# Kernel tuning notes

Hardware: AMD Instinct MI355X
Metric: run time of the kernel (lower is better)

Reference implementation:

```python
import jax, jax.numpy as jnp
import numpy as np


def setup_inputs() -> dict:
    key = jax.random.key(0)
    ks = jax.random.split(key, 10)
    N, CZ, CH = 512, 128, 128
    s = 1.0 / np.sqrt(CZ)  # keep pre-sigmoid activations in a sane range
    return {
        "z": jax.random.normal(ks[0], (N, N, CZ), dtype=jnp.float32),
        "mask": jnp.ones((N, N, 1), dtype=jnp.float32),
        "weight_ag": jax.random.normal(ks[1], (CH, CZ), dtype=jnp.float32) * s,
        "bias_ag": jax.random.normal(ks[2], (CH,), dtype=jnp.float32) * 0.02,
        "weight_ap": jax.random.normal(ks[3], (CH, CZ), dtype=jnp.float32) * s,
        "bias_ap": jax.random.normal(ks[4], (CH,), dtype=jnp.float32) * 0.02,
        "weight_bg": jax.random.normal(ks[5], (CH, CZ), dtype=jnp.float32) * s,
        "bias_bg": jax.random.normal(ks[6], (CH,), dtype=jnp.float32) * 0.02,
        "weight_bp": jax.random.normal(ks[7], (CH, CZ), dtype=jnp.float32) * s,
        "bias_bp": jax.random.normal(ks[8], (CH,), dtype=jnp.float32) * 0.02,
        "chunk_size": 32,
    }


def _triangle_mul(z, mask, w_ag, b_ag, w_ap, b_ap, w_bg, b_bg, w_bp, b_bp):
    # z: [N, N, c_z]; mask: [N, N, 1]; weights: [c, c_z]
    # a = mask * sigmoid(Linear_ag(z)) * Linear_ap(z)   -> [N, N, c]
    a = mask * jax.nn.sigmoid(jnp.einsum("ijz,cz->ijc", z, w_ag) + b_ag) * (
        jnp.einsum("ijz,cz->ijc", z, w_ap) + b_ap
    )
    b = mask * jax.nn.sigmoid(jnp.einsum("ijz,cz->ijc", z, w_bg) + b_bg) * (
        jnp.einsum("ijz,cz->ijc", z, w_bp) + b_bp
    )
    # outgoing triangle multiplicative combination, channel-first output [c, N, N]
    return jnp.einsum("ikc,jkc->cij", a, b)


def reference(z, mask, weight_ag, bias_ag, weight_ap, bias_ap,
              weight_bg, bias_bg, weight_bp, bias_bp, chunk_size):
    # The torch wrapper chunks the hidden-channel dim of the weights and
    # concatenates the per-chunk [c, N, N] outputs along dim 0. Since every
    # channel is independent, this is mathematically identical to running the
    # full computation at once; we do that (clean, fused form).
    return _triangle_mul(z, mask, weight_ag, bias_ag, weight_ap, bias_ap,
                         weight_bg, bias_bg, weight_bp, bias_bp)
```

## Files before the change

kernel.cpp:

```cpp
#include <hip/hip_runtime.h>
#include <stdint.h>


#define NDIM 512
#define CZ   128
#define CH   128
#define NPOS (NDIM * NDIM)
#define NTILE 16
#define POSB  (NTILE * 32)

typedef __attribute__((ext_vector_type(8))) __bf16 bf16x8;
typedef __attribute__((ext_vector_type(4))) float  f32x4;

__device__ __forceinline__ unsigned short f2bf(float f) {
  unsigned int u = __builtin_bit_cast(unsigned int, f);
  unsigned int r = (u + 0x7fffu + ((u >> 16) & 1u)) >> 16;
  return (unsigned short)r;
}

__global__ __launch_bounds__(256) void conv_weights(
    const float* __restrict__ wag, const float* __restrict__ wap,
    const float* __restrict__ wbg, const float* __restrict__ wbp,
    unsigned short* __restrict__ wbf) {
  int idx = blockIdx.x * 256 + threadIdx.x;
  int proj = idx >> 14;
  int rem  = idx & 16383;
  const float* src = (proj == 0) ? wag : (proj == 1) ? wap : (proj == 2) ? wbg : wbp;
  wbf[idx] = f2bf(src[rem]);
}

__global__ __launch_bounds__(256, 3) void proj_fuse(
    const float* __restrict__ z,
    const float* __restrict__ mask,
    const unsigned short* __restrict__ wbf,
    const float* __restrict__ bias_ag, const float* __restrict__ bias_ap,
    const float* __restrict__ bias_bg, const float* __restrict__ bias_bp,
    unsigned short* __restrict__ a_ws,
    unsigned short* __restrict__ b_ws) {
  __shared__ unsigned short zbuf[2][32 * 136];

  const int t    = threadIdx.x;
  const int lane = t & 63;
  const int w    = t >> 6;
  const int pair = blockIdx.y;
  const int base = blockIdx.x * POSB;

  const int ml    = lane & 15;
  const int q     = lane >> 4;
  const int koffl = q * 8;
  const int pg = pair * 2, pp = pg + 1;

  bf16x8 wg[4][2], wp[4][2];
#pragma unroll
  for (int ks = 0; ks < 4; ++ks)
#pragma unroll
    for (int ni = 0; ni < 2; ++ni) {
      const int c = w * 32 + ni * 16 + ml;
      wg[ks][ni] = *(const bf16x8*)&wbf[((size_t)pg * CH + c) * CZ + ks * 32 + koffl];
      wp[ks][ni] = *(const bf16x8*)&wbf[((size_t)pp * CH + c) * CZ + ks * 32 + koffl];
    }

  const float* bgp = pair ? bias_bg : bias_ag;
  const float* bpp = pair ? bias_bp : bias_ap;
  float bg[2], bp[2];
#pragma unroll
  for (int ni = 0; ni < 2; ++ni) {
    bg[ni] = bgp[w * 32 + ni * 16 + ml];
    bp[ni] = bpp[w * 32 + ni * 16 + ml];
  }
  unsigned short* plane = pair ? b_ws : a_ws;

  auto STAGE = [&](int b, int tt) {
    const int m0s = base + tt * 32;
#pragma unroll
    for (int it = 0; it < 4; ++it) {
      const int id  = it * 256 + t;
      const int row = id >> 5;
      const int c4  = id & 31;
      const float4 v = *(const float4*)(z + (size_t)(m0s + row) * CZ + c4 * 4);
      unsigned int lo = (unsigned int)f2bf(v.x) | ((unsigned int)f2bf(v.y) << 16);
      unsigned int hi = (unsigned int)f2bf(v.z) | ((unsigned int)f2bf(v.w) << 16);
      *(uint2*)&zbuf[b][row * 136 + c4 * 4] = make_uint2(lo, hi);
    }
  };

  STAGE(0, 0);
  __syncthreads();

#pragma unroll 1
  for (int tt = 0; tt < NTILE; ++tt) {
    const int m0 = base + tt * 32;
    const int cb = tt & 1;
    if (tt + 1 < NTILE) STAGE(cb ^ 1, tt + 1);

    f32x4 ag_[2][2], ap_[2][2];
#pragma unroll
    for (int mi = 0; mi < 2; ++mi)
#pragma unroll
      for (int ni = 0; ni < 2; ++ni) {
        ag_[mi][ni] = (f32x4){0.f, 0.f, 0.f, 0.f};
        ap_[mi][ni] = (f32x4){0.f, 0.f, 0.f, 0.f};
      }

#pragma unroll
    for (int ks = 0; ks < 4; ++ks) {
      bf16x8 af0 = *(const bf16x8*)&zbuf[cb][(ml)      * 136 + ks * 32 + koffl];
      bf16x8 af1 = *(const bf16x8*)&zbuf[cb][(ml + 16) * 136 + ks * 32 + koffl];
#pragma unroll
      for (int ni = 0; ni < 2; ++ni) {
        ag_[0][ni] = __builtin_amdgcn_mfma_f32_16x16x32_bf16(af0, wg[ks][ni], ag_[0][ni], 0, 0, 0);
        ag_[1][ni] = __builtin_amdgcn_mfma_f32_16x16x32_bf16(af1, wg[ks][ni], ag_[1][ni], 0, 0, 0);
        ap_[0][ni] = __builtin_amdgcn_mfma_f32_16x16x32_bf16(af0, wp[ks][ni], ap_[0][ni], 0, 0, 0);
        ap_[1][ni] = __builtin_amdgcn_mfma_f32_16x16x32_bf16(af1, wp[ks][ni], ap_[1][ni], 0, 0, 0);
      }
    }

#pragma unroll
    for (int mi = 0; mi < 2; ++mi) {
      const int pos0 = mi * 16 + q * 4;
      const float4 mv = *(const float4*)(mask + m0 + pos0);
      const float mr[4] = {mv.x, mv.y, mv.z, mv.w};
#pragma unroll
      for (int ni = 0; ni < 2; ++ni) {
        const int c = w * 32 + ni * 16 + ml;
        unsigned short h[4];
#pragma unroll
        for (int r = 0; r < 4; ++r) {
          const float g = ag_[mi][ni][r] + bg[ni];
          const float p = ap_[mi][ni][r] + bp[ni];
          const float s = 1.0f / (1.0f + __expf(-g));
          h[r] = f2bf(mr[r] * s * p);
        }
        *(uint2*)(plane + (size_t)c * NPOS + m0 + pos0) =
            make_uint2((unsigned int)h[0] | ((unsigned int)h[1] << 16),
                       (unsigned int)h[2] | ((unsigned int)h[3] << 16));
      }
    }
    __syncthreads();
  }
}

__global__ __launch_bounds__(256, 2) void tri_gemm(
    const unsigned short* __restrict__ a_ws,
    const unsigned short* __restrict__ b_ws,
    float* __restrict__ out) {
  __shared__ unsigned short sA[2][128 * 64];
  __shared__ unsigned short sB[2][128 * 64];

  const int t = threadIdx.x, lane = t & 63, wave = t >> 6;
  const int wm = wave >> 1, wn = wave & 1;

  const int L    = blockIdx.x;
  const int xcd  = L & 7;
  const int slot = L >> 3;
  const int c    = xcd * 16 + (slot >> 4);
  const int tile = slot & 15;
  const int ti   = tile >> 2, tj = tile & 3;
  const int i0 = ti * 128, j0 = tj * 128;

  const unsigned short* Ap = a_ws + (size_t)c * NPOS + (size_t)i0 * NDIM;
  const unsigned short* Bp = b_ws + (size_t)c * NPOS + (size_t)j0 * NDIM;

  f32x4 acc[4][4];
#pragma unroll
  for (int mi = 0; mi < 4; ++mi)
#pragma unroll
    for (int ni = 0; ni < 4; ++ni) acc[mi][ni] = (f32x4){0.f, 0.f, 0.f, 0.f};

  const int srow8  = t >> 3;
  const int schunk = t & 7;
  const int mrow = wm * 64 + (lane & 15);
  const int nrow = wn * 64 + (lane & 15);

  auto STAGE = [&](int b, int kk) {
    const int k0 = kk * 64;
#pragma unroll
    for (int i = 0; i < 4; ++i) {
      const int row = i * 32 + srow8;
      const int kcs = schunk ^ (row & 7);
      __builtin_amdgcn_global_load_lds(
          (const __attribute__((address_space(1))) unsigned int*)(Ap + (size_t)row * NDIM + k0 + kcs * 8),
          (__attribute__((address_space(3))) unsigned int*)&sA[b][(i * 256 + t) * 8], 16, 0, 0);
      __builtin_amdgcn_global_load_lds(
          (const __attribute__((address_space(1))) unsigned int*)(Bp + (size_t)row * NDIM + k0 + kcs * 8),
          (__attribute__((address_space(3))) unsigned int*)&sB[b][(i * 256 + t) * 8], 16, 0, 0);
    }
  };

  STAGE(0, 0);
  __syncthreads();

#pragma unroll 1
  for (int kk = 0; kk < 8; ++kk) {
    const int cur = kk & 1;
    if (kk < 7) STAGE(cur ^ 1, kk + 1);

#pragma unroll
    for (int ksub = 0; ksub < 2; ++ksub) {
      const int kc = ksub * 4 + (lane >> 4);
      bf16x8 af[4], bfr[4];
#pragma unroll
      for (int mi = 0; mi < 4; ++mi) {
        const int r = mrow + mi * 16;
        af[mi] = *(const bf16x8*)&sA[cur][r * 64 + ((kc ^ (r & 7)) << 3)];
      }
#pragma unroll
      for (int ni = 0; ni < 4; ++ni) {
        const int r = nrow + ni * 16;
        bfr[ni] = *(const bf16x8*)&sB[cur][r * 64 + ((kc ^ (r & 7)) << 3)];
      }
#pragma unroll
      for (int mi = 0; mi < 4; ++mi)
#pragma unroll
        for (int ni = 0; ni < 4; ++ni)
          acc[mi][ni] = __builtin_amdgcn_mfma_f32_16x16x32_bf16(af[mi], bfr[ni], acc[mi][ni], 0, 0, 0);
    }
    __syncthreads();
  }

  float* O = out + (size_t)c * NPOS + (size_t)i0 * NDIM + j0;
#pragma unroll
  for (int mi = 0; mi < 4; ++mi)
#pragma unroll
    for (int r = 0; r < 4; ++r) {
      const int m = wm * 64 + mi * 16 + (lane >> 4) * 4 + r;
#pragma unroll
      for (int ni = 0; ni < 4; ++ni) {
        const int n = wn * 64 + ni * 16 + (lane & 15);
        O[(size_t)m * NDIM + n] = acc[mi][ni][r];
      }
    }
}

extern "C" void kernel_launch(void* const* d_in, const int* in_sizes, int n_in,
                              void* d_out, int out_size, void* d_ws, size_t ws_size,
                              hipStream_t stream) {
  const float* z    = (const float*)d_in[0];
  const float* mask = (const float*)d_in[1];
  const float* wag  = (const float*)d_in[2];
  const float* bag  = (const float*)d_in[3];
  const float* wap  = (const float*)d_in[4];
  const float* bap  = (const float*)d_in[5];
  const float* wbg  = (const float*)d_in[6];
  const float* bbg  = (const float*)d_in[7];
  const float* wbp  = (const float*)d_in[8];
  const float* bbp  = (const float*)d_in[9];
  float* out = (float*)d_out;

  unsigned short* wbf  = (unsigned short*)d_ws;
  unsigned short* a_ws = (unsigned short*)((char*)d_ws + 131072);
  unsigned short* b_ws = (unsigned short*)((char*)d_ws + 131072 + (size_t)CH * NPOS * 2);

  conv_weights<<<dim3(256), dim3(256), 0, stream>>>(wag, wap, wbg, wbp, wbf);
  proj_fuse<<<dim3(NPOS / POSB, 2), dim3(256), 0, stream>>>(
      z, mask, wbf, bag, bap, bbg, bbp, a_ws, b_ws);
  tri_gemm<<<dim3(2048), dim3(256), 0, stream>>>(a_ws, b_ws, out);
}
```

Baseline: 382.9 us.

## Register-stage z loads, use hardware bf16 packing, single-buffer tri_gemm for occupancy

In proj_fuse, global z loads for the next tile now go into registers, and the bf16 conversion and LDS write happen after the epilogue, which hides load latency behind the MFMAs. Software bf16 rounding is replaced with v_cvt_pk_bf16_f32, and the sigmoid divide is replaced with a hardware reciprocal. In tri_gemm the LDS double buffer becomes a single buffer with load-then-sync, and launch bounds are raised to 3 blocks per CU. This trades prefetch overlap for occupancy. It also adds a potential hazard: the next iteration's LDS writes can race with reads still in progress unless a trailing barrier is kept.

Result: faster. 374.1 us (-2.3%).

```diff
diff --git a/kernel.cpp b/kernel.cpp
--- a/kernel.cpp
+++ b/kernel.cpp
@@ -16,6 +16,11 @@
   unsigned int u = __builtin_bit_cast(unsigned int, f);
   unsigned int r = (u + 0x7fffu + ((u >> 16) & 1u)) >> 16;
   return (unsigned short)r;
+}
+__device__ __forceinline__ unsigned int cvt_pk_bf16(float lo, float hi) {
+  unsigned int r;
+  asm("v_cvt_pk_bf16_f32 %0, %1, %2" : "=v"(r) : "v"(lo), "v"(hi));
+  return r;
 }
 
 __global__ __launch_bounds__(256) void conv_weights(
@@ -59,6 +64,13 @@
       wg[ks][ni] = *(const bf16x8*)&wbf[((size_t)pg * CH + c) * CZ + ks * 32 + koffl];
       wp[ks][ni] = *(const bf16x8*)&wbf[((size_t)pp * CH + c) * CZ + ks * 32 + koffl];
     }
+#pragma unroll
+  for (int ks = 0; ks < 4; ++ks)
+#pragma unroll
+    for (int ni = 0; ni < 2; ++ni) {
+      asm volatile("" : "+v"(wg[ks][ni]));
+      asm volatile("" : "+v"(wp[ks][ni]));
+    }
 
   const float* bgp = pair ? bias_bg : bias_ag;
   const float* bpp = pair ? bias_bp : bias_ap;
@@ -70,28 +82,34 @@
   }
   unsigned short* plane = pair ? b_ws : a_ws;
 
-  auto STAGE = [&](int b, int tt) {
+  float4 stg[4];
+  auto STAGE_LOAD = [&](int tt) {
     const int m0s = base + tt * 32;
 #pragma unroll
     for (int it = 0; it < 4; ++it) {
       const int id  = it * 256 + t;
-      const int row = id >> 5;
-      const int c4  = id & 31;
-      const float4 v = *(const float4*)(z + (size_t)(m0s + row) * CZ + c4 * 4);
-      unsigned int lo = (unsigned int)f2bf(v.x) | ((unsigned int)f2bf(v.y) << 16);
-      unsigned int hi = (unsigned int)f2bf(v.z) | ((unsigned int)f2bf(v.w) << 16);
-      *(uint2*)&zbuf[b][row * 136 + c4 * 4] = make_uint2(lo, hi);
+      stg[it] = *(const float4*)(z + (size_t)(m0s + (id >> 5)) * CZ + (id & 31) * 4);
     }
   };
-
-  STAGE(0, 0);
+  auto STAGE_WRITE = [&](int b) {
+#pragma unroll
+    for (int it = 0; it < 4; ++it) {
+      const int id = it * 256 + t;
+      *(uint2*)&zbuf[b][(id >> 5) * 136 + (id & 31) * 4] =
+          make_uint2(cvt_pk_bf16(stg[it].x, stg[it].y),
+                     cvt_pk_bf16(stg[it].z, stg[it].w));
+    }
+  };
+
+  STAGE_LOAD(0);
+  STAGE_WRITE(0);
   __syncthreads();
 
 #pragma unroll 1
   for (int tt = 0; tt < NTILE; ++tt) {
     const int m0 = base + tt * 32;
     const int cb = tt & 1;
-    if (tt + 1 < NTILE) STAGE(cb ^ 1, tt + 1);
+    if (tt + 1 < NTILE) STAGE_LOAD(tt + 1);
 
     f32x4 ag_[2][2], ap_[2][2];
 #pragma unroll
@@ -123,29 +141,30 @@
 #pragma unroll
       for (int ni = 0; ni < 2; ++ni) {
         const int c = w * 32 + ni * 16 + ml;
-        unsigned short h[4];
+        float v[4];
 #pragma unroll
         for (int r = 0; r < 4; ++r) {
           const float g = ag_[mi][ni][r] + bg[ni];
           const float p = ap_[mi][ni][r] + bp[ni];
-          const float s = 1.0f / (1.0f + __expf(-g));
-          h[r] = f2bf(mr[r] * s * p);
+          const float s = __builtin_amdgcn_rcpf(1.0f + __expf(-g));
+          v[r] = mr[r] * s * p;
         }
         *(uint2*)(plane + (size_t)c * NPOS + m0 + pos0) =
-            make_uint2((unsigned int)h[0] | ((unsigned int)h[1] << 16),
-                       (unsigned int)h[2] | ((unsigned int)h[3] << 16));
-      }
-    }
+            make_uint2(cvt_pk_bf16(v[0], v[1]), cvt_pk_bf16(v[2], v[3]));
+      }
+    }
+
+    if (tt + 1 < NTILE) STAGE_WRITE(cb ^ 1);
     __syncthreads();
   }
 }
 
-__global__ __launch_bounds__(256, 2) void tri_gemm(
+__global__ __launch_bounds__(256, 3) void tri_gemm(
     const unsigned short* __restrict__ a_ws,
     const unsigned short* __restrict__ b_ws,
     float* __restrict__ out) {
-  __shared__ unsigned short sA[2][128 * 64];
-  __shared__ unsigned short sB[2][128 * 64];
+  __shared__ unsigned short sA[128 * 64];
+  __shared__ unsigned short sB[128 * 64];
 
   const int t = threadIdx.x, lane = t & 63, wave = t >> 6;
   const int wm = wave >> 1, wn = wave & 1;
@@ -172,7 +191,7 @@
   const int mrow = wm * 64 + (lane & 15);
   const int nrow = wn * 64 + (lane & 15);
 
-  auto STAGE = [&](int b, int kk) {
+  for (int kk = 0; kk < 8; ++kk) {
     const int k0 = kk * 64;
 #pragma unroll
     for (int i = 0; i < 4; ++i) {
@@ -180,20 +199,12 @@
       const int kcs = schunk ^ (row & 7);
       __builtin_amdgcn_global_load_lds(
           (const __attribute__((address_space(1))) unsigned int*)(Ap + (size_t)row * NDIM + k0 + kcs * 8),
-          (__attribute__((address_space(3))) unsigned int*)&sA[b][(i * 256 + t) * 8], 16, 0, 0);
+          (__attribute__((address_space(3))) unsigned int*)&sA[(i * 256 + t) * 8], 16, 0, 0);
       __builtin_amdgcn_global_load_lds(
           (const __attribute__((address_space(1))) unsigned int*)(Bp + (size_t)row * NDIM + k0 + kcs * 8),
-          (__attribute__((address_space(3))) unsigned int*)&sB[b][(i * 256 + t) * 8], 16, 0, 0);
-    }
-  };
-
-  STAGE(0, 0);
-  __syncthreads();
-
-#pragma unroll 1
-  for (int kk = 0; kk < 8; ++kk) {
-    const int cur = kk & 1;
-    if (kk < 7) STAGE(cur ^ 1, kk + 1);
+          (__attribute__((address_space(3))) unsigned int*)&sB[(i * 256 + t) * 8], 16, 0, 0);
+    }
+    __syncthreads();
 
 #pragma unroll
     for (int ksub = 0; ksub < 2; ++ksub) {
@@ -202,12 +213,12 @@
 #pragma unroll
       for (int mi = 0; mi < 4; ++mi) {
         const int r = mrow + mi * 16;
-        af[mi] = *(const bf16x8*)&sA[cur][r * 64 + ((kc ^ (r & 7)) << 3)];
+        af[mi] = *(const bf16x8*)&sA[r * 64 + ((kc ^ (r & 7)) << 3)];
       }
 #pragma unroll
       for (int ni = 0; ni < 4; ++ni) {
         const int r = nrow + ni * 16;
-        bfr[ni] = *(const bf16x8*)&sB[cur][r * 64 + ((kc ^ (r & 7)) << 3)];
+        bfr[ni] = *(const bf16x8*)&sB[r * 64 + ((kc ^ (r & 7)) << 3)];
       }
 #pragma unroll
       for (int mi = 0; mi < 4; ++mi)
```
